# Optimization experiments

Hardware: AMD Instinct MI355X
Metric: run time of the kernel (lower is better)

Reference implementation:

```python
import jax, jax.numpy as jnp
import numpy as np

# Dims per init_kwargs
B, C_IN, H, W = 64, 512, 28, 28
GROWTH, BN_SIZE = 32, 4
C_MID = BN_SIZE * GROWTH  # 128
EPS = 1e-5
NUM_BITS = 8          # activation & weight quantization bits
NUM_CHUNKS = 16       # RangeBN chunking (eladhoffer quantize.py default)


def quantize(x, num_bits):
    """Uniform min/max quantize-dequantize (UniformQuantize forward)."""
    mn = x.min()
    mx = x.max()
    qmax = 2.0 ** num_bits - 1.0
    scale = jnp.maximum((mx - mn) / qmax, 1e-8)
    q = jnp.round((jnp.clip(x, mn, mx) - mn) / scale)
    return q * scale + mn


def conv2d(x, w, pad):
    return jax.lax.conv_general_dilated(
        x, w, window_strides=(1, 1), padding=[(pad, pad), (pad, pad)],
        dimension_numbers=('NCHW', 'OIHW', 'NCHW'))


def batchnorm2d(x, w, b):
    # training-mode BN: batch statistics over (N,H,W), biased variance
    mean = x.mean(axis=(0, 2, 3), keepdims=True)
    var = x.var(axis=(0, 2, 3), keepdims=True)
    xhat = (x - mean) * jax.lax.rsqrt(var + EPS)
    return xhat * w.reshape(1, -1, 1, 1) + b.reshape(1, -1, 1, 1)


def range_bn(x, w, b):
    # Range-based BN (training-mode): per-channel mean, scale from chunked min/max range
    Bx, Cx, Hx, Wx = x.shape
    y = x.transpose(1, 0, 2, 3).reshape(Cx, NUM_CHUNKS, -1)  # [C, chunks, n]
    mean_max = y.max(-1).mean(-1)   # [C]
    mean_min = y.min(-1).mean(-1)   # [C]
    mean = y.reshape(Cx, -1).mean(-1)  # [C]
    n = y.shape[-1]
    scale_fix = (0.5 * 0.35) * (1.0 + (np.pi * np.log(4.0)) ** 0.5) / ((2.0 * np.log(float(n))) ** 0.5)
    scale = 1.0 / ((mean_max - mean_min) * scale_fix + EPS)
    out = (x - mean.reshape(1, Cx, 1, 1)) * scale.reshape(1, Cx, 1, 1)
    qw = quantize(w, NUM_BITS)
    qb = quantize(b, NUM_BITS)
    return out * qw.reshape(1, Cx, 1, 1) + qb.reshape(1, Cx, 1, 1)


def setup_inputs() -> dict:
    key = jax.random.key(0)
    ks = jax.random.split(key, 7)
    x = jax.random.normal(ks[0], (B, C_IN, H, W), dtype=jnp.float32)
    bn1_w = jax.random.uniform(ks[1], (C_IN,), dtype=jnp.float32, minval=0.5, maxval=1.5)
    bn1_b = jax.random.normal(ks[2], (C_IN,), dtype=jnp.float32) * 0.1
    conv1_w = jax.random.normal(ks[3], (C_MID, C_IN, 1, 1), dtype=jnp.float32) * (2.0 / C_IN) ** 0.5
    rbn_w = jax.random.uniform(ks[4], (C_MID,), dtype=jnp.float32, minval=0.5, maxval=1.5)
    rbn_b = jax.random.normal(ks[5], (C_MID,), dtype=jnp.float32) * 0.1
    conv2_w = jax.random.normal(ks[6], (GROWTH, C_MID, 3, 3), dtype=jnp.float32) * (2.0 / (9 * C_MID)) ** 0.5
    return {"x": x, "bn1_w": bn1_w, "bn1_b": bn1_b, "conv1_w": conv1_w,
            "rbn_w": rbn_w, "rbn_b": rbn_b, "conv2_w": conv2_w}


def reference(x, bn1_w, bn1_b, conv1_w, rbn_w, rbn_b, conv2_w):
    # norm1 -> relu1 -> QConv2d(1x1) -> RangeBN -> relu2 -> QConv2d(3x3) -> concat
    h = jax.nn.relu(batchnorm2d(x, bn1_w, bn1_b))
    h = conv2d(quantize(h, NUM_BITS), quantize(conv1_w, NUM_BITS), pad=0)
    h = jax.nn.relu(range_bn(h, rbn_w, rbn_b))
    h = conv2d(quantize(h, NUM_BITS), quantize(conv2_w, NUM_BITS), pad=1)
    # drop_rate = 0 -> dropout is identity
    return jnp.concatenate([x, h], axis=1)
```

## Files before the change

### kernel.cpp

```cpp
#include <hip/hip_runtime.h>
#include <math.h>

static constexpr int BB    = 64;
static constexpr int C_IN  = 512;
static constexpr int C_MID = 128;
static constexpr int C_OUT = 32;
static constexpr int C_TOT = 544;
static constexpr int HW    = 784;

static constexpr size_t H2_OFF    = 0;
static constexpr size_t QW1_OFF   = 6422528;
static constexpr size_t QW2_OFF   = QW1_OFF + 65536;
static constexpr size_t PSTAT_OFF = QW2_OFF + 49152;
static constexpr size_t BNA_OFF   = PSTAT_OFF + 16384;
static constexpr size_t BNB_OFF   = BNA_OFF + 512;
static constexpr size_t A2_OFF    = BNB_OFF + 512;
static constexpr size_t B2_OFF    = A2_OFF + 128;
static constexpr size_t QRW_OFF   = B2_OFF + 128;
static constexpr size_t QRB_OFF   = QRW_OFF + 128;
static constexpr size_t SCAL_OFF  = QRB_OFF + 128;
static constexpr size_t PART_OFF  = SCAL_OFF + 16;
static constexpr size_t RP_OFF    = PART_OFF + 128;
static constexpr size_t PART2_OFF = RP_OFF + 172032;

#define DEVFN __device__ __forceinline__

typedef __bf16 bf16x8 __attribute__((ext_vector_type(8)));
typedef float  f32x4  __attribute__((ext_vector_type(4)));

DEVFN float qact(float v, float mn, float mx, float inv, float sc) {
    v = fminf(fmaxf(v, mn), mx);
    return fmaf(rintf((v - mn) * inv), sc, mn);
}

DEVFN unsigned f2bf(float f) {
    unsigned u = __float_as_uint(f);
    return (u + 0x7fffu + ((u >> 16) & 1u)) >> 16;
}

DEVFN float bf2f(unsigned short h) { return __uint_as_float((unsigned)h << 16); }

__global__ __launch_bounds__(256) void k_stats(const float* __restrict__ x,
                                               const float* __restrict__ conv1_w,
                                               const float* __restrict__ conv2_w,
                                               float* __restrict__ ws) {
    const int bid = blockIdx.x, tid = threadIdx.x;
    __shared__ float r0[256], r1[256], r2[256], r3[256];

    if (bid < 4096) {
        const int c = bid >> 3, bg = bid & 7;
        float s = 0.f, s2 = 0.f, mn = INFINITY, mx = -INFINITY;
        for (int i = tid; i < 1568; i += 256) {
            const int b = bg * 8 + i / 196, j = i % 196;
            const float4 v = ((const float4*)(x + ((size_t)b * C_IN + c) * HW))[j];
            s  += (v.x + v.y) + (v.z + v.w);
            s2 += v.x * v.x + v.y * v.y + v.z * v.z + v.w * v.w;
            mn = fminf(mn, fminf(fminf(v.x, v.y), fminf(v.z, v.w)));
            mx = fmaxf(mx, fmaxf(fmaxf(v.x, v.y), fmaxf(v.z, v.w)));
        }
        r0[tid] = s; r1[tid] = s2; r2[tid] = mn; r3[tid] = mx;
        __syncthreads();
        for (int off = 128; off > 0; off >>= 1) {
            if (tid < off) {
                r0[tid] += r0[tid + off];
                r1[tid] += r1[tid + off];
                r2[tid] = fminf(r2[tid], r2[tid + off]);
                r3[tid] = fmaxf(r3[tid], r3[tid + off]);
            }
            __syncthreads();
        }
        if (tid == 0) {
            float* p = ws + PSTAT_OFF + ((size_t)c * 8 + bg) * 4;
            p[0] = r0[0]; p[1] = r1[0]; p[2] = r2[0]; p[3] = r3[0];
        }
    } else {
        float mn = INFINITY, mx = -INFINITY;
        if (bid < 4128) {
            const float4* src = (const float4*)conv1_w + (size_t)(bid - 4096) * 512;
            for (int i = tid; i < 512; i += 256) {
                const float4 v = src[i];
                mn = fminf(mn, fminf(fminf(v.x, v.y), fminf(v.z, v.w)));
                mx = fmaxf(mx, fmaxf(fmaxf(v.x, v.y), fmaxf(v.z, v.w)));
            }
        } else {
            const float4* src = (const float4*)conv2_w + (size_t)(bid - 4128) * 1152;
            for (int i = tid; i < 1152; i += 256) {
                const float4 v = src[i];
                mn = fminf(mn, fminf(fminf(v.x, v.y), fminf(v.z, v.w)));
                mx = fmaxf(mx, fmaxf(fmaxf(v.x, v.y), fmaxf(v.z, v.w)));
            }
        }
        r2[tid] = mn; r3[tid] = mx;
        __syncthreads();
        for (int off = 128; off > 0; off >>= 1) {
            if (tid < off) { r2[tid] = fminf(r2[tid], r2[tid + off]); r3[tid] = fmaxf(r3[tid], r3[tid + off]); }
            __syncthreads();
        }
        if (tid == 0) {
            float* p = (bid < 4128) ? ws + PART_OFF + (size_t)(bid - 4096) * 2
                                    : ws + PART_OFF + 64 + (size_t)(bid - 4128) * 2;
            p[0] = r2[0]; p[1] = r3[0];
        }
    }
}

__global__ __launch_bounds__(256) void k_prep(const float* __restrict__ conv1_w,
                                              const float* __restrict__ conv2_w,
                                              const float* __restrict__ bn1_w,
                                              const float* __restrict__ bn1_b,
                                              const float* __restrict__ rbn_w,
                                              const float* __restrict__ rbn_b,
                                              float* __restrict__ ws) {
    const int b = blockIdx.x, tid = threadIdx.x;
    __shared__ float ra[256], rb[256];
    __shared__ float s_mn, s_sc;

    if (b < 32) {
        ra[tid] = tid < 32 ? ws[PART_OFF + tid * 2] : INFINITY;
        rb[tid] = tid < 32 ? ws[PART_OFF + tid * 2 + 1] : -INFINITY;
        __syncthreads();
        for (int off = 128; off > 0; off >>= 1) {
            if (tid < off) { ra[tid] = fminf(ra[tid], ra[tid + off]); rb[tid] = fmaxf(rb[tid], rb[tid + off]); }
            __syncthreads();
        }
        if (tid == 0) { s_mn = ra[0]; s_sc = fmaxf((rb[0] - ra[0]) / 255.f, 1e-8f); }
        __syncthreads();
        const float mnw = s_mn, scw = s_sc;
        unsigned short* qw = (unsigned short*)(ws + QW1_OFF);
        const int base = b * 2048;
#pragma unroll
        for (int t = 0; t < 8; ++t) {
            const int i = base + t * 256 + tid;
            const int co = i >> 9, k = i & 511;
            const float v = conv1_w[i];
            const float qv = fmaf(rintf((v - mnw) / scw), scw, mnw);
            const int ks = k >> 6, kc = (k >> 3) & 7, klo = k & 7;
            qw[(((size_t)ks * 128 + co) << 6) + (((kc ^ (co & 7)) << 3) | klo)] = (unsigned short)f2bf(qv);
        }
    } else if (b < 40) {
        ra[tid] = tid < 8 ? ws[PART_OFF + 64 + tid * 2] : INFINITY;
        rb[tid] = tid < 8 ? ws[PART_OFF + 64 + tid * 2 + 1] : -INFINITY;
        __syncthreads();
        for (int off = 128; off > 0; off >>= 1) {
            if (tid < off) { ra[tid] = fminf(ra[tid], ra[tid + off]); rb[tid] = fmaxf(rb[tid], rb[tid + off]); }
            __syncthreads();
        }
        if (tid == 0) { s_mn = ra[0]; s_sc = fmaxf((rb[0] - ra[0]) / 255.f, 1e-8f); }
        __syncthreads();
        const float mnw = s_mn, scw = s_sc;
        unsigned short* qw2 = (unsigned short*)(ws + QW2_OFF);
        const int base = (b - 32) * 4608;
        for (int i2 = tid; i2 < 4608; i2 += 256) {
            const int i = base + i2;
            const int co = i / 1152, r = i % 1152, ci = r / 9, tap = r % 9;
            const float v = conv2_w[i];
            const float qv = fmaf(rintf((v - mnw) / scw), scw, mnw);
            qw2[(size_t)co * 1152 + tap * 128 + ci] = (unsigned short)f2bf(qv);
        }
    } else if (b == 40) {
        float lmn = INFINITY, lmx = -INFINITY;
        for (int c = tid; c < 512; c += 256) {
            const float* p = ws + PSTAT_OFF + (size_t)c * 32;
            float s = 0.f, s2 = 0.f, cmn = INFINITY, cmx = -INFINITY;
            for (int g = 0; g < 8; ++g) {
                s += p[g * 4 + 0]; s2 += p[g * 4 + 1];
                cmn = fminf(cmn, p[g * 4 + 2]); cmx = fmaxf(cmx, p[g * 4 + 3]);
            }
            const float n = 50176.f;
            const float mean = s / n;
            const float var  = s2 / n - mean * mean;
            const float rstd = rsqrtf(var + 1e-5f);
            const float A  = rstd * bn1_w[c];
            const float Bc = bn1_b[c] - mean * A;
            ws[BNA_OFF + c] = A; ws[BNB_OFF + c] = Bc;
            const float v1 = A * cmn + Bc, v2 = A * cmx + Bc;
            lmn = fminf(lmn, fmaxf(0.f, fminf(v1, v2)));
            lmx = fmaxf(lmx, fmaxf(0.f, fmaxf(v1, v2)));
        }
        ra[tid] = lmn; rb[tid] = lmx;
        __syncthreads();
        for (int off = 128; off > 0; off >>= 1) {
            if (tid < off) { ra[tid] = fminf(ra[tid], ra[tid + off]); rb[tid] = fmaxf(rb[tid], rb[tid + off]); }
            __syncthreads();
        }
        if (tid == 0) {
            const float mn1 = ra[0], mx1 = rb[0];
            const float sc = fmaxf((mx1 - mn1) / 255.f, 1e-8f);
            ws[SCAL_OFF + 0] = mn1; ws[SCAL_OFF + 1] = sc; ws[SCAL_OFF + 2] = 1.f / sc; ws[SCAL_OFF + 6] = mx1;
        }
    } else {
        for (int which = 0; which < 2; ++which) {
            const float* src = which ? rbn_b : rbn_w;
            const size_t dst = which ? QRB_OFF : QRW_OFF;
            float v = 0.f;
            ra[tid] = INFINITY; rb[tid] = -INFINITY;
            if (tid < 128) { v = src[tid]; ra[tid] = v; rb[tid] = v; }
            __syncthreads();
            for (int off = 128; off > 0; off >>= 1) {
                if (tid < off) { ra[tid] = fminf(ra[tid], ra[tid + off]); rb[tid] = fmaxf(rb[tid], rb[tid + off]); }
                __syncthreads();
            }
            if (tid == 0) { s_mn = ra[0]; s_sc = fmaxf((rb[0] - ra[0]) / 255.f, 1e-8f); }
            __syncthreads();
            if (tid < 128) ws[dst + tid] = fmaf(rintf((v - s_mn) / s_sc), s_sc, s_mn);
            __syncthreads();
        }
    }
}

__global__ __launch_bounds__(256, 3) void k_conv1(const float* __restrict__ x,
                                                  float* __restrict__ out,
                                                  float* __restrict__ ws) {
    __shared__ __align__(16) unsigned short wt[64 * 64];
    __shared__ __align__(16) unsigned short ht[112 * 64];
    const int tid = threadIdx.x;
    const int pt = blockIdx.x, b = blockIdx.y, ch = blockIdx.z;
    const int p0 = pt * 112;
    const float mn1 = ws[SCAL_OFF + 0], sc1 = ws[SCAL_OFF + 1];
    const float inv1 = ws[SCAL_OFF + 2], mx1 = ws[SCAL_OFF + 6];
    const unsigned short* qw1 = (const unsigned short*)(ws + QW1_OFF);
    const float* xb = x + (size_t)b * C_IN * HW;
    float* outb = out + (size_t)b * C_TOT * HW;

    const int o = tid & 7, q = tid >> 3;
    const int wv = tid >> 6, g = (tid >> 4) & 3, r4 = tid & 15;

    f32x4 acc[7];
#pragma unroll
    for (int j = 0; j < 7; ++j) acc[j] = f32x4{0.f, 0.f, 0.f, 0.f};

    for (int ks = 0; ks < 8; ++ks) {
        const float4* wsrc = (const float4*)(qw1 + (((size_t)ks * 128 + (size_t)ch * 64) << 6));
        float4* wdst = (float4*)wt;
        wdst[tid] = wsrc[tid];
        wdst[tid + 256] = wsrc[tid + 256];

        if (tid < 224) {
            const int ci0 = ks * 64 + o * 8;
            float vv[8][4];
#pragma unroll
            for (int j = 0; j < 8; ++j) {
                const f32x4 v = *(const f32x4*)(xb + (size_t)(ci0 + j) * HW + p0 + q * 4);
                if (ch == 0)
                    __builtin_nontemporal_store(v, (f32x4*)(outb + (size_t)(ci0 + j) * HW + p0 + q * 4));
                const float A = ws[BNA_OFF + ci0 + j], Bc = ws[BNB_OFF + ci0 + j];
                vv[j][0] = qact(fmaxf(0.f, fmaf(v.x, A, Bc)), mn1, mx1, inv1, sc1);
                vv[j][1] = qact(fmaxf(0.f, fmaf(v.y, A, Bc)), mn1, mx1, inv1, sc1);
                vv[j][2] = qact(fmaxf(0.f, fmaf(v.z, A, Bc)), mn1, mx1, inv1, sc1);
                vv[j][3] = qact(fmaxf(0.f, fmaf(v.w, A, Bc)), mn1, mx1, inv1, sc1);
            }
#pragma unroll
            for (int r = 0; r < 4; ++r) {
                const int p = q * 4 + r;
                uint4 pk;
                pk.x = f2bf(vv[0][r]) | (f2bf(vv[1][r]) << 16);
                pk.y = f2bf(vv[2][r]) | (f2bf(vv[3][r]) << 16);
                pk.z = f2bf(vv[4][r]) | (f2bf(vv[5][r]) << 16);
                pk.w = f2bf(vv[6][r]) | (f2bf(vv[7][r]) << 16);
                *(uint4*)&ht[p * 64 + ((o ^ (p & 7)) << 3)] = pk;
            }
        }
        __syncthreads();

#pragma unroll
        for (int ksub = 0; ksub < 2; ++ksub) {
            const int kk = ksub * 4 + g;
            const int col = wv * 16 + r4;
            const bf16x8 af = *(const bf16x8*)&wt[col * 64 + ((kk ^ (col & 7)) << 3)];
            bf16x8 bfr[7];
#pragma unroll
            for (int pf = 0; pf < 7; ++pf) {
                const int p = pf * 16 + r4;
                bfr[pf] = *(const bf16x8*)&ht[p * 64 + ((kk ^ (p & 7)) << 3)];
            }
#pragma unroll
            for (int pf = 0; pf < 7; ++pf)
                acc[pf] = __builtin_amdgcn_mfma_f32_16x16x32_bf16(af, bfr[pf], acc[pf], 0, 0, 0);
        }
        __syncthreads();
    }

    unsigned short* hb = (unsigned short*)(ws + H2_OFF) + (size_t)b * C_MID * HW;
    const int co0 = ch * 64 + wv * 16 + g * 4;
#pragma unroll
    for (int pf = 0; pf < 7; ++pf) {
        const int p = p0 + pf * 16 + r4;
#pragma unroll
        for (int r = 0; r < 4; ++r)
            hb[(size_t)(co0 + r) * HW + p] = (unsigned short)f2bf(acc[pf][r]);
    }

#pragma unroll
    for (int r = 0; r < 4; ++r) {
        float s = 0.f, mn = INFINITY, mx = -INFINITY;
#pragma unroll
        for (int pf = 0; pf < 7; ++pf) {
            const float v = acc[pf][r];
            s += v; mn = fminf(mn, v); mx = fmaxf(mx, v);
        }
#pragma unroll
        for (int m = 1; m < 16; m <<= 1) {
            s  += __shfl_xor(s, m, 64);
            mn  = fminf(mn, __shfl_xor(mn, m, 64));
            mx  = fmaxf(mx, __shfl_xor(mx, m, 64));
        }
        if (r4 == 0) {
            const int co = co0 + r;
            float* dst = ws + RP_OFF + (((size_t)co * 64 + b) * 7 + pt) * 3;
            dst[0] = s; dst[1] = mn; dst[2] = mx;
        }
    }
}

__global__ __launch_bounds__(64) void k_rbn_combine(float* __restrict__ ws) {
    const int c = blockIdx.x, t = threadIdx.x;
    const int ch = t >> 2, sub = t & 3;
    const int b = ch * 4 + sub;
    const float* rp = ws + RP_OFF + ((size_t)c * 64 + b) * 21;
    float s = 0.f, mn = INFINITY, mx = -INFINITY;
#pragma unroll
    for (int pt = 0; pt < 7; ++pt) {
        s += rp[pt * 3 + 0];
        mn = fminf(mn, rp[pt * 3 + 1]);
        mx = fmaxf(mx, rp[pt * 3 + 2]);
    }
#pragma unroll
    for (int m = 1; m < 4; m <<= 1) {
        s  += __shfl_xor(s, m, 64);
        mn  = fminf(mn, __shfl_xor(mn, m, 64));
        mx  = fmaxf(mx, __shfl_xor(mx, m, 64));
    }
    float smx = mx, smn = mn, stot = s, gmn = mn, gmx = mx;
#pragma unroll
    for (int m = 4; m < 64; m <<= 1) {
        smx  += __shfl_xor(smx, m, 64);
        smn  += __shfl_xor(smn, m, 64);
        stot += __shfl_xor(stot, m, 64);
        gmn   = fminf(gmn, __shfl_xor(gmn, m, 64));
        gmx   = fmaxf(gmx, __shfl_xor(gmx, m, 64));
    }
    if (t == 0) {
        const float mm = smx * (1.f / 16.f), mnm = smn * (1.f / 16.f);
        const float mean = stot / 50176.f;
        const double PI_D = 3.14159265358979323846;
        const double sfd = 0.175 * (1.0 + sqrt(PI_D * log(4.0))) / sqrt(2.0 * log(3136.0));
        const float scale = 1.f / ((mm - mnm) * (float)sfd + 1e-5f);
        const float A  = scale * ws[QRW_OFF + c];
        const float Bc = ws[QRB_OFF + c] - mean * A;
        ws[A2_OFF + c] = A; ws[B2_OFF + c] = Bc;
        const float v1 = A * gmn + Bc, v2 = A * gmx + Bc;
        ws[PART2_OFF + c * 2 + 0] = fmaxf(0.f, fminf(v1, v2));
        ws[PART2_OFF + c * 2 + 1] = fmaxf(0.f, fmaxf(v1, v2));
    }
}

__global__ __launch_bounds__(256, 2) void k_conv2(float* __restrict__ out, const float* __restrict__ ws) {
    __shared__ __align__(16) unsigned short lact[7 * 30 * 128];
    __shared__ float sra[128], srb[128];
    __shared__ float s_mn3, s_mx3, s_sc3, s_inv3;
    const int tid = threadIdx.x;
    const int pt = blockIdx.x, b = blockIdx.y;
    const int y0 = pt * 4;

    if (tid < 128) { sra[tid] = ws[PART2_OFF + tid * 2]; srb[tid] = ws[PART2_OFF + tid * 2 + 1]; }
    __syncthreads();
    for (int off = 64; off > 0; off >>= 1) {
        if (tid < off) { sra[tid] = fminf(sra[tid], sra[tid + off]); srb[tid] = fmaxf(srb[tid], srb[tid + off]); }
        __syncthreads();
    }
    if (tid == 0) {
        const float mn3 = sra[0], mx3 = srb[0];
        const float sc = fmaxf((mx3 - mn3) / 255.f, 1e-8f);
        s_mn3 = mn3; s_mx3 = mx3; s_sc3 = sc; s_inv3 = 1.f / sc;
    }
    {
        const uint4 z = {0u, 0u, 0u, 0u};
        uint4* lp = (uint4*)lact;
        for (int i = tid; i < 3360; i += 256) lp[i] = z;
    }
    __syncthreads();
    const float mn3 = s_mn3, mx3 = s_mx3, sc3 = s_sc3, inv3 = s_inv3;

    const unsigned short* h2b = (const unsigned short*)(ws + H2_OFF) + (size_t)b * C_MID * HW;
    for (int task = tid; task < 672; task += 256) {
        const int oct = task / 42, rem = task % 42, r = rem / 7, xq = rem % 7;
        const int gy = y0 - 1 + r;
        if (gy < 0 || gy > 27) continue;
        float vv[8][4];
#pragma unroll
        for (int j = 0; j < 8; ++j) {
            const int ci = oct * 8 + j;
            const ushort4 v = *(const ushort4*)(h2b + (size_t)ci * HW + gy * 28 + xq * 4);
            const float A = ws[A2_OFF + ci], Bc = ws[B2_OFF + ci];
            vv[j][0] = qact(fmaxf(0.f, fmaf(bf2f(v.x), A, Bc)), mn3, mx3, inv3, sc3);
            vv[j][1] = qact(fmaxf(0.f, fmaf(bf2f(v.y), A, Bc)), mn3, mx3, inv3, sc3);
            vv[j][2] = qact(fmaxf(0.f, fmaf(bf2f(v.z), A, Bc)), mn3, mx3, inv3, sc3);
            vv[j][3] = qact(fmaxf(0.f, fmaf(bf2f(v.w), A, Bc)), mn3, mx3, inv3, sc3);
        }
#pragma unroll
        for (int xi = 0; xi < 4; ++xi) {
            const int col = xq * 4 + xi + 1;
            const int phys = (oct + col) & 15;
            uint4 pk;
            pk.x = f2bf(vv[0][xi]) | (f2bf(vv[1][xi]) << 16);
            pk.y = f2bf(vv[2][xi]) | (f2bf(vv[3][xi]) << 16);
            pk.z = f2bf(vv[4][xi]) | (f2bf(vv[5][xi]) << 16);
            pk.w = f2bf(vv[6][xi]) | (f2bf(vv[7][xi]) << 16);
            *(uint4*)&lact[((r * 30 + col) * 16 + phys) * 8] = pk;
        }
    }
    __syncthreads();

    const int wv = tid >> 6, lane = tid & 63, r4 = lane & 15, g = lane >> 4;
    int py[2], px[2];
#pragma unroll
    for (int i = 0; i < 2; ++i) {
        const int p = (wv * 2 + i) * 16 + r4;
        py[i] = p / 28; px[i] = p % 28;
    }
    f32x4 acc[2][2];
#pragma unroll
    for (int ct = 0; ct < 2; ++ct)
#pragma unroll
        for (int i = 0; i < 2; ++i) acc[ct][i] = f32x4{0.f, 0.f, 0.f, 0.f};

    const unsigned short* qw2 = (const unsigned short*)(ws + QW2_OFF);
    for (int tap = 0; tap < 9; ++tap) {
        const int dy = tap / 3, dx = tap % 3;
        bf16x8 afr[2][4];
#pragma unroll
        for (int ct = 0; ct < 2; ++ct)
#pragma unroll
            for (int c4 = 0; c4 < 4; ++c4) {
                const int co = ct * 16 + r4;
                afr[ct][c4] = *(const bf16x8*)&qw2[(size_t)co * 1152 + tap * 128 + c4 * 32 + g * 8];
            }
#pragma unroll
        for (int c4 = 0; c4 < 4; ++c4) {
            bf16x8 bfr[2];
#pragma unroll
            for (int i = 0; i < 2; ++i) {
                const int row = py[i] + dy, col = px[i] + dx;
                const int phys = (c4 * 4 + g + col) & 15;
                bfr[i] = *(const bf16x8*)&lact[((row * 30 + col) * 16 + phys) * 8];
            }
#pragma unroll
            for (int ct = 0; ct < 2; ++ct)
#pragma unroll
                for (int i = 0; i < 2; ++i)
                    acc[ct][i] = __builtin_amdgcn_mfma_f32_16x16x32_bf16(afr[ct][c4], bfr[i], acc[ct][i], 0, 0, 0);
        }
    }

#pragma unroll
    for (int ct = 0; ct < 2; ++ct)
#pragma unroll
        for (int i = 0; i < 2; ++i) {
            const int pf = wv * 2 + i;
            if (pf < 7) {
                const int p = pf * 16 + r4;
#pragma unroll
                for (int r = 0; r < 4; ++r) {
                    const int co = ct * 16 + g * 4 + r;
                    out[((size_t)b * C_TOT + 512 + co) * HW + y0 * 28 + p] = acc[ct][i][r];
                }
            }
        }
}

extern "C" void kernel_launch(void* const* d_in, const int* in_sizes, int n_in,
                              void* d_out, int out_size, void* d_ws, size_t ws_size,
                              hipStream_t stream) {
    const float* x       = (const float*)d_in[0];
    const float* bn1_w   = (const float*)d_in[1];
    const float* bn1_b   = (const float*)d_in[2];
    const float* conv1_w = (const float*)d_in[3];
    const float* rbn_w   = (const float*)d_in[4];
    const float* rbn_b   = (const float*)d_in[5];
    const float* conv2_w = (const float*)d_in[6];
    float* out = (float*)d_out;
    float* ws  = (float*)d_ws;

    k_stats<<<4136, 256, 0, stream>>>(x, conv1_w, conv2_w, ws);
    k_prep<<<42, 256, 0, stream>>>(conv1_w, conv2_w, bn1_w, bn1_b, rbn_w, rbn_b, ws);
    k_conv1<<<dim3(7, 64, 2), 256, 0, stream>>>(x, out, ws);
    k_rbn_combine<<<128, 64, 0, stream>>>(ws);
    k_conv2<<<dim3(7, 64), 256, 0, stream>>>(out, ws);
}
```

Before: 123.7 us.

## Compute all 128 conv1 output channels per block and prefetch next x slice

The conv1 kernel no longer splits output channels across two blocks; each block now computes all 128 channels, so x is read and BN/quantized once instead of twice. It also register-prefetches the next 64-channel x slice during the current iteration and simplifies the activation quantize by dropping the upper clamp. The costs are doubled accumulator registers, a larger weight tile in shared memory, lower occupancy (launch bound 2), and half as many blocks in the grid.

New measurement: 104.4 us. -15.6%, faster.

```diff
diff --git a/kernel.cpp b/kernel.cpp
--- a/kernel.cpp
+++ b/kernel.cpp
@@ -208,16 +208,16 @@
     }
 }
 
-__global__ __launch_bounds__(256, 3) void k_conv1(const float* __restrict__ x,
+__global__ __launch_bounds__(256, 2) void k_conv1(const float* __restrict__ x,
                                                   float* __restrict__ out,
                                                   float* __restrict__ ws) {
-    __shared__ __align__(16) unsigned short wt[64 * 64];
+    __shared__ __align__(16) unsigned short wt[128 * 64];
     __shared__ __align__(16) unsigned short ht[112 * 64];
     const int tid = threadIdx.x;
-    const int pt = blockIdx.x, b = blockIdx.y, ch = blockIdx.z;
+    const int pt = blockIdx.x, b = blockIdx.y;
     const int p0 = pt * 112;
     const float mn1 = ws[SCAL_OFF + 0], sc1 = ws[SCAL_OFF + 1];
-    const float inv1 = ws[SCAL_OFF + 2], mx1 = ws[SCAL_OFF + 6];
+    const float inv1 = ws[SCAL_OFF + 2];
     const unsigned short* qw1 = (const unsigned short*)(ws + QW1_OFF);
     const float* xb = x + (size_t)b * C_IN * HW;
     float* outb = out + (size_t)b * C_TOT * HW;
@@ -225,29 +225,43 @@
     const int o = tid & 7, q = tid >> 3;
     const int wv = tid >> 6, g = (tid >> 4) & 3, r4 = tid & 15;
 
-    f32x4 acc[7];
-#pragma unroll
-    for (int j = 0; j < 7; ++j) acc[j] = f32x4{0.f, 0.f, 0.f, 0.f};
+    f32x4 acc[2][7];
+#pragma unroll
+    for (int i = 0; i < 2; ++i)
+#pragma unroll
+        for (int j = 0; j < 7; ++j) acc[i][j] = f32x4{0.f, 0.f, 0.f, 0.f};
+
+    f32x4 xreg[8];
+    if (tid < 224) {
+#pragma unroll
+        for (int j = 0; j < 8; ++j)
+            xreg[j] = *(const f32x4*)(xb + (size_t)(o * 8 + j) * HW + p0 + q * 4);
+    }
 
     for (int ks = 0; ks < 8; ++ks) {
-        const float4* wsrc = (const float4*)(qw1 + (((size_t)ks * 128 + (size_t)ch * 64) << 6));
+        const float4* wsrc = (const float4*)(qw1 + (size_t)ks * 8192);
         float4* wdst = (float4*)wt;
-        wdst[tid] = wsrc[tid];
-        wdst[tid + 256] = wsrc[tid + 256];
+#pragma unroll
+        for (int i = 0; i < 4; ++i) wdst[tid + i * 256] = wsrc[tid + i * 256];
 
         if (tid < 224) {
             const int ci0 = ks * 64 + o * 8;
             float vv[8][4];
 #pragma unroll
             for (int j = 0; j < 8; ++j) {
-                const f32x4 v = *(const f32x4*)(xb + (size_t)(ci0 + j) * HW + p0 + q * 4);
-                if (ch == 0)
-                    __builtin_nontemporal_store(v, (f32x4*)(outb + (size_t)(ci0 + j) * HW + p0 + q * 4));
+                const f32x4 v = xreg[j];
+                __builtin_nontemporal_store(v, (f32x4*)(outb + (size_t)(ci0 + j) * HW + p0 + q * 4));
                 const float A = ws[BNA_OFF + ci0 + j], Bc = ws[BNB_OFF + ci0 + j];
-                vv[j][0] = qact(fmaxf(0.f, fmaf(v.x, A, Bc)), mn1, mx1, inv1, sc1);
-                vv[j][1] = qact(fmaxf(0.f, fmaf(v.y, A, Bc)), mn1, mx1, inv1, sc1);
-                vv[j][2] = qact(fmaxf(0.f, fmaf(v.z, A, Bc)), mn1, mx1, inv1, sc1);
-                vv[j][3] = qact(fmaxf(0.f, fmaf(v.w, A, Bc)), mn1, mx1, inv1, sc1);
+                vv[j][0] = fmaf(rintf((fmaxf(fmaf(v.x, A, Bc), 0.f) - mn1) * inv1), sc1, mn1);
+                vv[j][1] = fmaf(rintf((fmaxf(fmaf(v.y, A, Bc), 0.f) - mn1) * inv1), sc1, mn1);
+                vv[j][2] = fmaf(rintf((fmaxf(fmaf(v.z, A, Bc), 0.f) - mn1) * inv1), sc1, mn1);
+                vv[j][3] = fmaf(rintf((fmaxf(fmaf(v.w, A, Bc), 0.f) - mn1) * inv1), sc1, mn1);
+            }
+            if (ks < 7) {
+                const int ci0n = (ks + 1) * 64 + o * 8;
+#pragma unroll
+                for (int j = 0; j < 8; ++j)
+                    xreg[j] = *(const f32x4*)(xb + (size_t)(ci0n + j) * HW + p0 + q * 4);
             }
 #pragma unroll
             for (int r = 0; r < 4; ++r) {
@@ -265,51 +279,61 @@
 #pragma unroll
         for (int ksub = 0; ksub < 2; ++ksub) {
             const int kk = ksub * 4 + g;
-            const int col = wv * 16 + r4;
-            const bf16x8 af = *(const bf16x8*)&wt[col * 64 + ((kk ^ (col & 7)) << 3)];
-            bf16x8 bfr[7];
+            bf16x8 af[2], bfr[7];
+#pragma unroll
+            for (int ct = 0; ct < 2; ++ct) {
+                const int co = wv * 32 + ct * 16 + r4;
+                af[ct] = *(const bf16x8*)&wt[co * 64 + ((kk ^ (co & 7)) << 3)];
+            }
 #pragma unroll
             for (int pf = 0; pf < 7; ++pf) {
                 const int p = pf * 16 + r4;
                 bfr[pf] = *(const bf16x8*)&ht[p * 64 + ((kk ^ (p & 7)) << 3)];
             }
 #pragma unroll
-            for (int pf = 0; pf < 7; ++pf)
-                acc[pf] = __builtin_amdgcn_mfma_f32_16x16x32_bf16(af, bfr[pf], acc[pf], 0, 0, 0);
+            for (int ct = 0; ct < 2; ++ct)
+#pragma unroll
+                for (int pf = 0; pf < 7; ++pf)
+                    acc[ct][pf] = __builtin_amdgcn_mfma_f32_16x16x32_bf16(af[ct], bfr[pf], acc[ct][pf], 0, 0, 0);
         }
         __syncthreads();
     }
 
     unsigned short* hb = (unsigned short*)(ws + H2_OFF) + (size_t)b * C_MID * HW;
-    const int co0 = ch * 64 + wv * 16 + g * 4;
-#pragma unroll
-    for (int pf = 0; pf < 7; ++pf) {
-        const int p = p0 + pf * 16 + r4;
-#pragma unroll
-        for (int r = 0; r < 4; ++r)
-            hb[(size_t)(co0 + r) * HW + p] = (unsigned short)f2bf(acc[pf][r]);
-    }
-
-#pragma unroll
-    for (int r = 0; r < 4; ++r) {
-        float s = 0.f, mn = INFINITY, mx = -INFINITY;
+#pragma unroll
+    for (int ct = 0; ct < 2; ++ct) {
+        const int co0 = wv * 32 + ct * 16 + g * 4;
 #pragma unroll
         for (int pf = 0; pf < 7; ++pf) {
-            const float v = acc[pf][r];
-            s += v; mn = fminf(mn, v); mx = fmaxf(mx, v);
-        }
-#pragma unroll
-        for (int m = 1; m < 16; m <<= 1) {
-            s  += __shfl_xor(s, m, 64);
-            mn  = fminf(mn, __shfl_xor(mn, m, 64));
-            mx  = fmaxf(mx, __shfl_xor(mx, m, 64));
-        }
-        if (r4 == 0) {
-            const int co = co0 + r;
-            float* dst = ws + RP_OFF + (((size_t)co * 64 + b) * 7 + pt) * 3;
-            dst[0] = s; dst[1] = mn; dst[2] = mx;
-        }
-    }
+            const int p = p0 + pf * 16 + r4;
+#pragma unroll
+            for (int r = 0; r < 4; ++r)
+                hb[(size_t)(co0 + r) * HW + p] = (unsigned short)f2bf(acc[ct][pf][r]);
+        }
+    }
+
+#pragma unroll
+    for (int ct = 0; ct < 2; ++ct)
+#pragma unroll
+        for (int r = 0; r < 4; ++r) {
+            float s = 0.f, mn = INFINITY, mx = -INFINITY;
+#pragma unroll
+            for (int pf = 0; pf < 7; ++pf) {
+                const float v = acc[ct][pf][r];
+                s += v; mn = fminf(mn, v); mx = fmaxf(mx, v);
+            }
+#pragma unroll
+            for (int m = 1; m < 16; m <<= 1) {
+                s  += __shfl_xor(s, m, 64);
+                mn  = fminf(mn, __shfl_xor(mn, m, 64));
+                mx  = fmaxf(mx, __shfl_xor(mx, m, 64));
+            }
+            if (r4 == 0) {
+                const int co = wv * 32 + ct * 16 + g * 4 + r;
+                float* dst = ws + RP_OFF + (((size_t)co * 64 + b) * 7 + pt) * 3;
+                dst[0] = s; dst[1] = mn; dst[2] = mx;
+            }
+        }
 }
 
 __global__ __launch_bounds__(64) void k_rbn_combine(float* __restrict__ ws) {
@@ -483,7 +507,7 @@
 
     k_stats<<<4136, 256, 0, stream>>>(x, conv1_w, conv2_w, ws);
     k_prep<<<42, 256, 0, stream>>>(conv1_w, conv2_w, bn1_w, bn1_b, rbn_w, rbn_b, ws);
-    k_conv1<<<dim3(7, 64, 2), 256, 0, stream>>>(x, out, ws);
+    k_conv1<<<dim3(7, 64), 256, 0, stream>>>(x, out, ws);
     k_rbn_combine<<<128, 64, 0, stream>>>(ws);
     k_conv2<<<dim3(7, 64), 256, 0, stream>>>(out, ws);
 }
```
